# Performance work log

Hardware: AMD Instinct MI355X
Metric: run time of the kernel (lower is better)

The kernel has to match this reference:

```python
import jax, jax.numpy as jnp
import numpy as np

N = 262144   # nodes
E = 4194304  # edges (avg degree 16)
G = 1024     # graphs in batch
F_IN, F_GCN, F_DENSE = 3, 16, 16
NEG_SLOPE = 0.01  # nn.LeakyReLU default


def _leaky(x):
    return jax.nn.leaky_relu(x, NEG_SLOPE)


def _gcn_conv(x, W, b, src, dst, ew):
    """PyG GCNConv: h = x @ W; symmetric deg-norm with self-loops (weight 1);
    out[i] = sum_{(j->i)} norm_e * h[j] + (1/deg_i) * h[i] + b."""
    h = x @ W                                   # [N, out]
    deg = jax.ops.segment_sum(ew, dst, num_segments=N) + 1.0  # +1 from self-loop
    dinv = jnp.where(deg > 0, jax.lax.rsqrt(deg), 0.0)        # deg^{-1/2}
    norm = dinv[src] * ew * dinv[dst]           # [E]
    agg = jax.ops.segment_sum(h[src] * norm[:, None], dst, num_segments=N)
    agg = agg + h * (dinv * dinv)[:, None]      # self-loop message, norm = 1/deg
    return agg + b


def setup_inputs() -> dict:
    key = jax.random.key(0)
    ks = jax.random.split(key, 24)
    inp = {
        "X": jax.random.normal(ks[0], (N, F_IN), dtype=jnp.float32),
        "Edge_index": jax.random.randint(ks[1], (2, E), 0, N, dtype=jnp.int64) if jax.config.jax_enable_x64 else jax.random.randint(ks[1], (2, E), 0, N, dtype=jnp.int32),
        "Edge_weight": jax.random.uniform(ks[2], (E,), dtype=jnp.float32),
        "Batching": jnp.sort(jax.random.randint(ks[3], (N,), 0, G, dtype=jnp.int32)),
        "num_graphs": G,
    }
    def lin(k, fi, fo):
        kw, kb = jax.random.split(k)
        s = 1.0 / np.sqrt(fi)
        return (jax.random.uniform(kw, (fi, fo), minval=-s, maxval=s, dtype=jnp.float32),
                jax.random.uniform(kb, (fo,), minval=-s, maxval=s, dtype=jnp.float32))
    inp["W1"], inp["b1"] = lin(ks[4], F_IN, F_GCN)
    inp["W2"], inp["b2"] = lin(ks[5], F_GCN, F_GCN)
    inp["Wp1"], inp["bp1"] = lin(ks[6], F_GCN, F_DENSE)
    inp["Wp2"], inp["bp2"] = lin(ks[7], F_DENSE, F_DENSE)
    inp["Wp3"], inp["bp3"] = lin(ks[8], F_DENSE, 2)
    inp["Wt1"], inp["bt1"] = lin(ks[9], F_GCN, F_DENSE)
    inp["Wt2"], inp["bt2"] = lin(ks[10], F_DENSE, F_DENSE)
    inp["Wt3"], inp["bt3"] = lin(ks[11], F_DENSE, 2)
    return inp


def reference(X, Edge_index, Edge_weight, Batching, num_graphs,
              W1, b1, W2, b2,
              Wp1, bp1, Wp2, bp2, Wp3, bp3,
              Wt1, bt1, Wt2, bt2, Wt3, bt3):
    src, dst = Edge_index[0], Edge_index[1]
    out = _leaky(_gcn_conv(X, W1, b1, src, dst, Edge_weight))
    out = _leaky(_gcn_conv(out, W2, b2, src, dst, Edge_weight))
    # global mean pool over graphs
    sums = jax.ops.segment_sum(out, Batching, num_segments=num_graphs)
    cnt = jax.ops.segment_sum(jnp.ones((out.shape[0],), out.dtype), Batching,
                              num_segments=num_graphs)
    pooled = sums / jnp.maximum(cnt, 1.0)[:, None]   # [G, 16]
    Phi = _leaky(pooled @ Wp1 + bp1)
    Phi = _leaky(Phi @ Wp2 + bp2)
    Phi = Phi @ Wp3 + bp3
    Theta = _leaky(pooled @ Wt1 + bt1)
    Theta = _leaky(Theta @ Wt2 + bt2)
    Theta = Theta @ Wt3 + bt3
    return jnp.concatenate((Phi, Theta), axis=1)   # [G, 4]
```

## Files before the change

### kernel.cpp

```cpp
#include <hip/hip_runtime.h>


#define NBUCK 512
#define BCAP  10240
#define CHUNK 4096
#define NTILE 8
#define TSH   15

__device__ __forceinline__ float leaky(float x) { return x > 0.f ? x : 0.01f * x; }

__global__ __launch_bounds__(256) void
binA_kernel(const int* __restrict__ src, const int* __restrict__ dst,
            const float* __restrict__ ew, int* __restrict__ bucketCursor,
            int2* __restrict__ coarse, int E) {
    __shared__ int lhist[NBUCK], lbase[NBUCK], lcur[NBUCK], gbase[NBUCK];
    __shared__ int tmp[256];
    __shared__ int2 stag[CHUNK];
    __shared__ unsigned short sbuck[CHUNK];
    int t = threadIdx.x;
    int base = blockIdx.x * CHUNK;
    for (int b = t; b < NBUCK; b += 256) { lhist[b] = 0; lcur[b] = 0; }
    __syncthreads();
    int n = min(CHUNK, E - base);
    int myDst[16], mySrc[16]; float myEw[16];
#pragma unroll
    for (int k = 0; k < 16; ++k) {
        int j = t + k * 256;
        if (j < n) {
            int d = dst[base + j];
            myDst[k] = d; mySrc[k] = src[base + j]; myEw[k] = ew[base + j];
            atomicAdd(&lhist[d >> 9], 1);
        } else myDst[k] = -1;
    }
    __syncthreads();
    tmp[t] = lhist[2 * t] + lhist[2 * t + 1];
    __syncthreads();
    for (int off = 1; off < 256; off <<= 1) {
        int v = (t >= off) ? tmp[t - off] : 0;
        __syncthreads();
        tmp[t] += v;
        __syncthreads();
    }
    int pb = (t == 0) ? 0 : tmp[t - 1];
    lbase[2 * t] = pb;
    lbase[2 * t + 1] = pb + lhist[2 * t];
    __syncthreads();
    for (int b = t; b < NBUCK; b += 256) {
        int c = lhist[b];
        gbase[b] = c ? atomicAdd(&bucketCursor[b], c) : 0;
    }
    for (int k = 0; k < 16; ++k) {
        int d = myDst[k];
        if (d >= 0) {
            int b = d >> 9;
            int p = lbase[b] + atomicAdd(&lcur[b], 1);
            stag[p] = make_int2(mySrc[k] | ((d & 511) << 18), __float_as_int(myEw[k]));
            sbuck[p] = (unsigned short)b;
        }
    }
    __syncthreads();
    for (int j = t; j < n; j += 256) {
        int b = sbuck[j];
        coarse[(size_t)b * BCAP + gbase[b] + (j - lbase[b])] = stag[j];
    }
}

__global__ void bscan_kernel(const int* __restrict__ bucketCursor,
                             int* __restrict__ bucketBase, int* __restrict__ row,
                             int N, int E) {
    __shared__ int s[NBUCK];
    int t = threadIdx.x;
    int v = bucketCursor[t];
    s[t] = v;
    __syncthreads();
    for (int off = 1; off < NBUCK; off <<= 1) {
        int x = (t >= off) ? s[t - off] : 0;
        __syncthreads();
        s[t] += x;
        __syncthreads();
    }
    bucketBase[t] = s[t] - v;
    if (t == 0) row[N] = E;
}

__global__ __launch_bounds__(512) void
binB_kernel(const int* __restrict__ bucketCursor, const int* __restrict__ bucketBase,
            const int2* __restrict__ coarse, int2* __restrict__ edata,
            int* __restrict__ row, float* __restrict__ dinv,
            uint4* __restrict__ tcnt) {
    __shared__ int loff[NBUCK * NTILE];
    __shared__ int lcur[NBUCK * NTILE];
    __shared__ int tmp[512];
    int b = blockIdx.x, t = threadIdx.x;
    for (int i = t; i < NBUCK * NTILE; i += 512) { loff[i] = 0; lcur[i] = 0; }
    __syncthreads();
    int cnt = bucketCursor[b];
    int gb  = bucketBase[b];
    const int2* cb = coarse + (size_t)b * BCAP;
    for (int j = t; j < cnt; j += 512) {
        int e = cb[j].x;
        atomicAdd(&loff[(((e >> 18) & 511) << 3) | ((e & 0x3FFFF) >> TSH)], 1);
    }
    __syncthreads();
    int base8 = t * 8, s = 0;
#pragma unroll
    for (int k = 0; k < 8; ++k) s += loff[base8 + k];
    tmp[t] = s;
    __syncthreads();
    for (int off = 1; off < 512; off <<= 1) {
        int v = (t >= off) ? tmp[t - off] : 0;
        __syncthreads();
        tmp[t] += v;
        __syncthreads();
    }
    int run = tmp[t] - s;
#pragma unroll
    for (int k = 0; k < 8; ++k) { int v = loff[base8 + k]; loff[base8 + k] = run; run += v; }
    __syncthreads();
    int o[9];
#pragma unroll
    for (int k = 0; k < 8; ++k) o[k] = loff[base8 + k];
    o[8] = (t == 511) ? cnt : loff[base8 + 8];
    int node = b * 512 + t;
    row[node] = gb + o[0];
    uint4 p;
    p.x = (unsigned)(o[1] - o[0]) | ((unsigned)(o[2] - o[1]) << 16);
    p.y = (unsigned)(o[3] - o[2]) | ((unsigned)(o[4] - o[3]) << 16);
    p.z = (unsigned)(o[5] - o[4]) | ((unsigned)(o[6] - o[5]) << 16);
    p.w = (unsigned)(o[7] - o[6]) | ((unsigned)(o[8] - o[7]) << 16);
    tcnt[node] = p;
    for (int j = t; j < cnt; j += 512) {
        int2 e = cb[j];
        int sv = e.x & 0x3FFFF;
        int key = (((e.x >> 18) & 511) << 3) | (sv >> TSH);
        int pos = gb + loff[key] + atomicAdd(&lcur[key], 1);
        edata[pos] = make_int2(sv, e.y);
    }
    __syncthreads();
    float dsum = 0.f;
    for (int j = gb + o[0], e1 = gb + o[8]; j < e1; ++j)
        dsum += __int_as_float(edata[j].y);
    dinv[node] = rsqrtf(1.0f + dsum);
}

__global__ void node1_kernel(const float* __restrict__ X, const float* __restrict__ W1,
                             const float* __restrict__ dinv, float* __restrict__ h, int N) {
    __shared__ float w[48];
    if (threadIdx.x < 48) w[threadIdx.x] = W1[threadIdx.x];
    __syncthreads();
    int i = blockIdx.x * blockDim.x + threadIdx.x;
    if (i >= N) return;
    float x0 = X[3 * i], x1 = X[3 * i + 1], x2 = X[3 * i + 2];
    float di = dinv[i];
    float4* hp = (float4*)(h + (size_t)i * 16);
#pragma unroll
    for (int k = 0; k < 4; ++k) {
        float4 v;
        v.x = (x0 * w[4 * k + 0] + x1 * w[16 + 4 * k + 0] + x2 * w[32 + 4 * k + 0]) * di;
        v.y = (x0 * w[4 * k + 1] + x1 * w[16 + 4 * k + 1] + x2 * w[32 + 4 * k + 1]) * di;
        v.z = (x0 * w[4 * k + 2] + x1 * w[16 + 4 * k + 2] + x2 * w[32 + 4 * k + 2]) * di;
        v.w = (x0 * w[4 * k + 3] + x1 * w[16 + 4 * k + 3] + x2 * w[32 + 4 * k + 3]) * di;
        hp[k] = v;
    }
}

__global__ __launch_bounds__(512) void
aggA_kernel(const int* __restrict__ row, const uint4* __restrict__ tcnt,
            const int2* __restrict__ edata, const float* __restrict__ dinv,
            const float* __restrict__ hprime, const float* __restrict__ b1,
            const float* __restrict__ W2, float* __restrict__ h2) {
    __shared__ float w[256];
    __shared__ float bb[16];
    __shared__ float sx[128][17];
    int t = threadIdx.x;
    if (t < 256) w[t] = W2[t];
    else if (t < 272) bb[t - 256] = b1[t - 256];
    int ln = t >> 2, l = t & 3;
    int iA = blockIdx.x * 256 + ln, iB = iA + 128;
    const float4* hp = (const float4*)hprime;
    int eA = row[iA], eB = row[iB];
    uint4 cAv = tcnt[iA], cBv = tcnt[iB];
    unsigned ca[4] = {cAv.x, cAv.y, cAv.z, cAv.w};
    unsigned cb[4] = {cBv.x, cBv.y, cBv.z, cBv.w};
    float diA = dinv[iA], diB = dinv[iB];
    float4 accA = hp[(size_t)iA * 4 + l];
    float4 accB = hp[(size_t)iB * 4 + l];
#pragma unroll
    for (int tt = 0; tt < NTILE; ++tt) {
        int nA = (ca[tt >> 1] >> ((tt & 1) * 16)) & 0xFFFF;
        int nB = (cb[tt >> 1] >> ((tt & 1) * 16)) & 0xFFFF;
        for (int e = eA + nA; eA < e; ++eA) {
            int2 ed = edata[eA];
            float ewv = __int_as_float(ed.y);
            float4 v = hp[(size_t)ed.x * 4 + l];
            accA.x += v.x * ewv; accA.y += v.y * ewv;
            accA.z += v.z * ewv; accA.w += v.w * ewv;
        }
        for (int e = eB + nB; eB < e; ++eB) {
            int2 ed = edata[eB];
            float ewv = __int_as_float(ed.y);
            float4 v = hp[(size_t)ed.x * 4 + l];
            accB.x += v.x * ewv; accB.y += v.y * ewv;
            accB.z += v.z * ewv; accB.w += v.w * ewv;
        }
        __syncthreads();
    }
    sx[ln][4 * l + 0] = leaky(diA * accA.x + bb[4 * l + 0]);
    sx[ln][4 * l + 1] = leaky(diA * accA.y + bb[4 * l + 1]);
    sx[ln][4 * l + 2] = leaky(diA * accA.z + bb[4 * l + 2]);
    sx[ln][4 * l + 3] = leaky(diA * accA.w + bb[4 * l + 3]);
    __syncthreads();
    {
        float a0 = 0.f, a1 = 0.f, a2 = 0.f, a3 = 0.f;
#pragma unroll
        for (int q = 0; q < 16; ++q) {
            float xv = sx[ln][q];
            a0 += xv * w[q * 16 + 4 * l + 0];
            a1 += xv * w[q * 16 + 4 * l + 1];
            a2 += xv * w[q * 16 + 4 * l + 2];
            a3 += xv * w[q * 16 + 4 * l + 3];
        }
        ((float4*)h2)[(size_t)iA * 4 + l] = make_float4(a0 * diA, a1 * diA, a2 * diA, a3 * diA);
    }
    __syncthreads();
    sx[ln][4 * l + 0] = leaky(diB * accB.x + bb[4 * l + 0]);
    sx[ln][4 * l + 1] = leaky(diB * accB.y + bb[4 * l + 1]);
    sx[ln][4 * l + 2] = leaky(diB * accB.z + bb[4 * l + 2]);
    sx[ln][4 * l + 3] = leaky(diB * accB.w + bb[4 * l + 3]);
    __syncthreads();
    {
        float a0 = 0.f, a1 = 0.f, a2 = 0.f, a3 = 0.f;
#pragma unroll
        for (int q = 0; q < 16; ++q) {
            float xv = sx[ln][q];
            a0 += xv * w[q * 16 + 4 * l + 0];
            a1 += xv * w[q * 16 + 4 * l + 1];
            a2 += xv * w[q * 16 + 4 * l + 2];
            a3 += xv * w[q * 16 + 4 * l + 3];
        }
        ((float4*)h2)[(size_t)iB * 4 + l] = make_float4(a0 * diB, a1 * diB, a2 * diB, a3 * diB);
    }
}

__global__ __launch_bounds__(512) void
aggB_kernel(const int* __restrict__ row, const uint4* __restrict__ tcnt,
            const int2* __restrict__ edata, const float* __restrict__ dinv,
            const float* __restrict__ h2prime, float* __restrict__ agg2) {
    int t = threadIdx.x;
    int ln = t >> 2, l = t & 3;
    int iA = blockIdx.x * 256 + ln, iB = iA + 128;
    const float4* hp = (const float4*)h2prime;
    int eA = row[iA], eB = row[iB];
    uint4 cAv = tcnt[iA], cBv = tcnt[iB];
    unsigned ca[4] = {cAv.x, cAv.y, cAv.z, cAv.w};
    unsigned cb[4] = {cBv.x, cBv.y, cBv.z, cBv.w};
    float diA = dinv[iA], diB = dinv[iB];
    float4 accA = hp[(size_t)iA * 4 + l];
    float4 accB = hp[(size_t)iB * 4 + l];
#pragma unroll
    for (int tt = 0; tt < NTILE; ++tt) {
        int nA = (ca[tt >> 1] >> ((tt & 1) * 16)) & 0xFFFF;
        int nB = (cb[tt >> 1] >> ((tt & 1) * 16)) & 0xFFFF;
        for (int e = eA + nA; eA < e; ++eA) {
            int2 ed = edata[eA];
            float ewv = __int_as_float(ed.y);
            float4 v = hp[(size_t)ed.x * 4 + l];
            accA.x += v.x * ewv; accA.y += v.y * ewv;
            accA.z += v.z * ewv; accA.w += v.w * ewv;
        }
        for (int e = eB + nB; eB < e; ++eB) {
            int2 ed = edata[eB];
            float ewv = __int_as_float(ed.y);
            float4 v = hp[(size_t)ed.x * 4 + l];
            accB.x += v.x * ewv; accB.y += v.y * ewv;
            accB.z += v.z * ewv; accB.w += v.w * ewv;
        }
        __syncthreads();
    }
    ((float4*)agg2)[(size_t)iA * 4 + l] =
        make_float4(accA.x * diA, accA.y * diA, accA.z * diA, accA.w * diA);
    ((float4*)agg2)[(size_t)iB * 4 + l] =
        make_float4(accB.x * diB, accB.y * diB, accB.z * diB, accB.w * diB);
}

__device__ void head_mlp(const float* pooled,
                         const float* __restrict__ Wa, const float* __restrict__ ba,
                         const float* __restrict__ Wb, const float* __restrict__ bb,
                         const float* __restrict__ Wc, const float* __restrict__ bc,
                         float* o) {
    float t[16], u[16];
#pragma unroll
    for (int f = 0; f < 16; ++f) {
        float a = ba[f];
        for (int k = 0; k < 16; ++k) a += pooled[k] * Wa[k * 16 + f];
        t[f] = leaky(a);
    }
#pragma unroll
    for (int f = 0; f < 16; ++f) {
        float a = bb[f];
        for (int k = 0; k < 16; ++k) a += t[k] * Wb[k * 16 + f];
        u[f] = leaky(a);
    }
    float o0 = bc[0], o1 = bc[1];
    for (int k = 0; k < 16; ++k) { o0 += u[k] * Wc[2 * k]; o1 += u[k] * Wc[2 * k + 1]; }
    o[0] = o0; o[1] = o1;
}

__global__ void pool_head_kernel(const float* __restrict__ agg2, const float* __restrict__ b2,
                                 const int* __restrict__ batching, int N,
                                 const float* __restrict__ Wp1, const float* __restrict__ bp1,
                                 const float* __restrict__ Wp2, const float* __restrict__ bp2,
                                 const float* __restrict__ Wp3, const float* __restrict__ bp3,
                                 const float* __restrict__ Wt1, const float* __restrict__ bt1,
                                 const float* __restrict__ Wt2, const float* __restrict__ bt2,
                                 const float* __restrict__ Wt3, const float* __restrict__ bt3,
                                 float* __restrict__ out) {
    int g = blockIdx.x;
    __shared__ int bounds[2];
    if (threadIdx.x < 2) {
        int v = g + (int)threadIdx.x;
        int lo = 0, hi = N;
        while (lo < hi) { int m = (lo + hi) >> 1; if (batching[m] < v) lo = m + 1; else hi = m; }
        bounds[threadIdx.x] = lo;
    }
    __syncthreads();
    int lo = bounds[0], hi = bounds[1];
    int f = threadIdx.x & 15, r = threadIdx.x >> 4;
    float bf = b2[f];
    float acc = 0.f;
    for (int i = lo + r; i < hi; i += 16) acc += leaky(agg2[(size_t)i * 16 + f] + bf);
    __shared__ float red[16][17];
    red[r][f] = acc;
    __syncthreads();
    __shared__ float pooled[16];
    if (r == 0) {
        float s = 0.f;
#pragma unroll
        for (int k = 0; k < 16; ++k) s += red[k][f];
        pooled[f] = s / fmaxf((float)(hi - lo), 1.0f);
    }
    __syncthreads();
    if (threadIdx.x == 0) {
        float o[2];
        head_mlp(pooled, Wp1, bp1, Wp2, bp2, Wp3, bp3, o);
        out[4 * g + 0] = o[0]; out[4 * g + 1] = o[1];
    } else if (threadIdx.x == 1) {
        float o[2];
        head_mlp(pooled, Wt1, bt1, Wt2, bt2, Wt3, bt3, o);
        out[4 * g + 2] = o[0]; out[4 * g + 3] = o[1];
    }
}

extern "C" void kernel_launch(void* const* d_in, const int* in_sizes, int n_in,
                              void* d_out, int out_size, void* d_ws, size_t ws_size,
                              hipStream_t stream) {
    const float* X        = (const float*)d_in[0];
    const int*   ei       = (const int*)d_in[1];
    const float* ew       = (const float*)d_in[2];
    const int*   batching = (const int*)d_in[3];
    const float* W1  = (const float*)d_in[5];  const float* b1  = (const float*)d_in[6];
    const float* W2  = (const float*)d_in[7];  const float* b2  = (const float*)d_in[8];
    const float* Wp1 = (const float*)d_in[9];  const float* bp1 = (const float*)d_in[10];
    const float* Wp2 = (const float*)d_in[11]; const float* bp2 = (const float*)d_in[12];
    const float* Wp3 = (const float*)d_in[13]; const float* bp3 = (const float*)d_in[14];
    const float* Wt1 = (const float*)d_in[15]; const float* bt1 = (const float*)d_in[16];
    const float* Wt2 = (const float*)d_in[17]; const float* bt2 = (const float*)d_in[18];
    const float* Wt3 = (const float*)d_in[19]; const float* bt3 = (const float*)d_in[20];

    const int N = in_sizes[3];
    const int E = in_sizes[2];
    const int G = out_size / 4;
    const int* src = ei;
    const int* dst = ei + E;

    char* ws = (char*)d_ws;
    size_t off = 0;
    int2*  edata = (int2*)(ws + off);  off += (size_t)E * 8;
    char*  regionA = ws + off;         off += (size_t)N * 64 * 3;
    int2*  coarse = (int2*)regionA;
    float* hprime = (float*)regionA;
    float* h2     = (float*)(regionA + (size_t)N * 64);
    float* agg2   = (float*)(regionA + (size_t)N * 128);
    int*   bucketCursor = (int*)(ws + off); off += NBUCK * 4;
    int*   bucketBase   = (int*)(ws + off); off += NBUCK * 4;
    int*   row   = (int*)(ws + off);   off += (size_t)(N + 4) * 4;
    float* dinv  = (float*)(ws + off); off += (size_t)N * 4;
    uint4* tcnt  = (uint4*)(ws + off); off += (size_t)N * 16;
    float* out   = (float*)d_out;

    hipMemsetAsync(bucketCursor, 0, NBUCK * 4, stream);

    const int tb = 256;
    binA_kernel<<<(E + CHUNK - 1) / CHUNK, tb, 0, stream>>>(src, dst, ew, bucketCursor, coarse, E);
    bscan_kernel<<<1, NBUCK, 0, stream>>>(bucketCursor, bucketBase, row, N, E);
    binB_kernel<<<NBUCK, 512, 0, stream>>>(bucketCursor, bucketBase, coarse, edata, row, dinv, tcnt);
    node1_kernel<<<(N + tb - 1) / tb, tb, 0, stream>>>(X, W1, dinv, hprime, N);
    aggA_kernel<<<N / 256, 512, 0, stream>>>(row, tcnt, edata, dinv, hprime, b1, W2, h2);
    aggB_kernel<<<N / 256, 512, 0, stream>>>(row, tcnt, edata, dinv, h2, agg2);
    pool_head_kernel<<<G, tb, 0, stream>>>(agg2, b2, batching, N,
                                           Wp1, bp1, Wp2, bp2, Wp3, bp3,
                                           Wt1, bt1, Wt2, bt2, Wt3, bt3, out);
}
```

Before: 429.6 us.

## Stage binB scatter in shared memory and cache coarse edges in registers

binB now reads each coarse edge once into registers, computes its key there, and scatters into a shared-memory staging array (BCAP int2 = 80KB) instead of scattering straight to global memory. The finished bucket is then written to global memory with coalesced stores. The degree sum is read from shared memory instead of global. It also drops the separate lcur array by reusing loff as the atomic cursor. The trade-off is higher LDS use and register pressure, since RCAP=20 per-thread edge slots are combined with launch_bounds(512,2). This can cut occupancy, and buckets with more than RCAP*512 edges would be silently dropped.

```diff
diff --git a/kernel.cpp b/kernel.cpp
--- a/kernel.cpp
+++ b/kernel.cpp
@@ -6,6 +6,7 @@
 #define CHUNK 4096
 #define NTILE 8
 #define TSH   15
+#define RCAP  20
 
 __device__ __forceinline__ float leaky(float x) { return x > 0.f ? x : 0.01f * x; }
 
@@ -83,23 +84,30 @@
     if (t == 0) row[N] = E;
 }
 
-__global__ __launch_bounds__(512) void
+__global__ __launch_bounds__(512, 2) void
 binB_kernel(const int* __restrict__ bucketCursor, const int* __restrict__ bucketBase,
             const int2* __restrict__ coarse, int2* __restrict__ edata,
             int* __restrict__ row, float* __restrict__ dinv,
             uint4* __restrict__ tcnt) {
+    __shared__ int2 sedata[BCAP];
     __shared__ int loff[NBUCK * NTILE];
-    __shared__ int lcur[NBUCK * NTILE];
     __shared__ int tmp[512];
     int b = blockIdx.x, t = threadIdx.x;
-    for (int i = t; i < NBUCK * NTILE; i += 512) { loff[i] = 0; lcur[i] = 0; }
+    for (int i = t; i < NBUCK * NTILE; i += 512) loff[i] = 0;
     __syncthreads();
     int cnt = bucketCursor[b];
     int gb  = bucketBase[b];
     const int2* cb = coarse + (size_t)b * BCAP;
-    for (int j = t; j < cnt; j += 512) {
-        int e = cb[j].x;
-        atomicAdd(&loff[(((e >> 18) & 511) << 3) | ((e & 0x3FFFF) >> TSH)], 1);
+    int2 myE[RCAP]; int myKey[RCAP];
+#pragma unroll
+    for (int k = 0; k < RCAP; ++k) {
+        int j = t + k * 512;
+        if (j < cnt) {
+            int2 e = cb[j];
+            myE[k] = e;
+            myKey[k] = (((e.x >> 18) & 511) << 3) | ((e.x & 0x3FFFF) >> TSH);
+            atomicAdd(&loff[myKey[k]], 1);
+        } else myKey[k] = -1;
     }
     __syncthreads();
     int base8 = t * 8, s = 0;
@@ -114,13 +122,11 @@
         __syncthreads();
     }
     int run = tmp[t] - s;
-#pragma unroll
-    for (int k = 0; k < 8; ++k) { int v = loff[base8 + k]; loff[base8 + k] = run; run += v; }
-    __syncthreads();
     int o[9];
 #pragma unroll
-    for (int k = 0; k < 8; ++k) o[k] = loff[base8 + k];
-    o[8] = (t == 511) ? cnt : loff[base8 + 8];
+    for (int k = 0; k < 8; ++k) { int v = loff[base8 + k]; o[k] = run; loff[base8 + k] = run; run += v; }
+    o[8] = run;
+    __syncthreads();
     int node = b * 512 + t;
     row[node] = gb + o[0];
     uint4 p;
@@ -129,17 +135,17 @@
     p.z = (unsigned)(o[5] - o[4]) | ((unsigned)(o[6] - o[5]) << 16);
     p.w = (unsigned)(o[7] - o[6]) | ((unsigned)(o[8] - o[7]) << 16);
     tcnt[node] = p;
-    for (int j = t; j < cnt; j += 512) {
-        int2 e = cb[j];
-        int sv = e.x & 0x3FFFF;
-        int key = (((e.x >> 18) & 511) << 3) | (sv >> TSH);
-        int pos = gb + loff[key] + atomicAdd(&lcur[key], 1);
-        edata[pos] = make_int2(sv, e.y);
-    }
-    __syncthreads();
+#pragma unroll
+    for (int k = 0; k < RCAP; ++k) {
+        if (myKey[k] >= 0) {
+            int pos = atomicAdd(&loff[myKey[k]], 1);
+            sedata[pos] = make_int2(myE[k].x & 0x3FFFF, myE[k].y);
+        }
+    }
+    __syncthreads();
+    for (int j = t; j < cnt; j += 512) edata[gb + j] = sedata[j];
     float dsum = 0.f;
-    for (int j = gb + o[0], e1 = gb + o[8]; j < e1; ++j)
-        dsum += __int_as_float(edata[j].y);
+    for (int j = o[0]; j < o[8]; ++j) dsum += __int_as_float(sedata[j].y);
     dinv[node] = rsqrtf(1.0f + dsum);
 }
 
```

After: 374.9 us. -12.7%, faster.
